# Kernel tuning notes

Measured on AMD Instinct MI355X. Metric: run time of the kernel, lower is better.

The kernel has to match this reference:

```python
import jax, jax.numpy as jnp
import numpy as np

B, S, D, H = 2, 2048, 1024, 16
HD = D // H  # head_dim = 64


def setup_inputs() -> dict:
    key = jax.random.key(0)
    ks = jax.random.split(key, 6)
    scale = D ** -0.5
    x = jax.random.normal(ks[0], (B, S, D), dtype=jnp.float32)
    wq = jax.random.normal(ks[1], (D, D), dtype=jnp.float32) * scale
    wk = jax.random.normal(ks[2], (D, D), dtype=jnp.float32) * scale
    wv = jax.random.normal(ks[3], (D, D), dtype=jnp.float32) * scale
    wo = jax.random.normal(ks[4], (D, D), dtype=jnp.float32) * scale
    # RoPE frequencies: theta_i = 10000^(-2i/HD), angles[t, i] = t * theta_i
    inv_freq = 1.0 / (10000.0 ** (np.arange(0, HD, 2, dtype=np.float32) / HD))
    t = np.arange(S, dtype=np.float32)
    angles = np.outer(t, inv_freq)  # [S, HD//2]
    freqs_cos = jnp.asarray(np.cos(angles), dtype=jnp.float32)
    freqs_sin = jnp.asarray(np.sin(angles), dtype=jnp.float32)
    # additive causal mask [1,1,S,S]
    neg = jnp.float32(-1e9)
    mask = jnp.triu(jnp.full((S, S), neg, dtype=jnp.float32), k=1)[None, None]
    return {"x": x, "wq": wq, "wk": wk, "wv": wv, "wo": wo,
            "freqs_cos": freqs_cos, "freqs_sin": freqs_sin,
            "mask": mask, "start_pos": 0}


def _apply_rope(q, freqs_cos, freqs_sin):
    # q: [B, S, H, HD] -> pairs (even, odd) rotated by angle per position
    b, s, h, hd = q.shape
    q2 = q.reshape(b, s, h, hd // 2, 2)
    qr, qi = q2[..., 0], q2[..., 1]
    c = freqs_cos[None, :, None, :]  # [1, S, 1, HD//2]
    sn = freqs_sin[None, :, None, :]
    out_r = qr * c - qi * sn
    out_i = qr * sn + qi * c
    return jnp.stack([out_r, out_i], axis=-1).reshape(b, s, h, hd)


def reference(x, wq, wk, wv, wo, freqs_cos, freqs_sin, mask, start_pos):
    b, s, _ = x.shape
    xq = (x @ wq).reshape(b, s, H, HD)
    xk = (x @ wk).reshape(b, s, H, HD)
    xv = (x @ wv).reshape(b, s, H, HD)
    xq = _apply_rope(xq, freqs_cos, freqs_sin)
    xk = _apply_rope(xk, freqs_cos, freqs_sin)
    # [B, H, S, HD]
    q = xq.transpose(0, 2, 1, 3)
    k = xk.transpose(0, 2, 1, 3)
    v = xv.transpose(0, 2, 1, 3)
    scores = jnp.einsum('bhqd,bhkd->bhqk', q, k) / jnp.sqrt(jnp.float32(HD))
    scores = scores + mask
    probs = jax.nn.softmax(scores.astype(jnp.float32), axis=-1).astype(q.dtype)
    out = jnp.einsum('bhqk,bhkd->bhqd', probs, v)
    out = out.transpose(0, 2, 1, 3).reshape(b, s, H * HD)
    return out @ wo
```

## Files before the change

kernel.cpp:

```cpp
#include <hip/hip_runtime.h>

typedef unsigned short u16;
typedef __bf16 bf16x8 __attribute__((ext_vector_type(8)));
typedef float f32x4 __attribute__((ext_vector_type(4)));

#define DD 1024
#define SS 2048
#define HH 16
#define HDIM 64

#define VMCNT(N) asm volatile("s_waitcnt vmcnt(" #N ")" ::: "memory")
#define LGKMCNT0 asm volatile("s_waitcnt lgkmcnt(0)" ::: "memory")
#define MEMFENCE asm volatile("" ::: "memory")
#define SBAR __builtin_amdgcn_s_barrier()

__device__ __forceinline__ u16 f2bf(float f) {
  union { float f; unsigned u; } x; x.f = f;
  unsigned r = x.u + 0x7FFFu + ((x.u >> 16) & 1u);
  return (u16)(r >> 16);
}

__device__ __forceinline__ u16 f2bf_s(float f) {
  unsigned r;
  asm("v_cvt_pk_bf16_f32 %0, %1, %2" : "=v"(r) : "v"(f), "v"(0.f));
  return (u16)r;
}

__device__ __forceinline__ void gload_lds16(const u16* g, u16* l) {
  __builtin_amdgcn_global_load_lds((const __attribute__((address_space(1))) void*)g,
                                   (__attribute__((address_space(3))) void*)l, 16, 0, 0);
}

__global__ __launch_bounds__(256) void prep(const float* __restrict__ x,
                                            const float* __restrict__ w0, const float* __restrict__ w1,
                                            const float* __restrict__ w2, const float* __restrict__ w3,
                                            u16* __restrict__ xb, u16* __restrict__ wT) {
  __shared__ float t[32][33];
  const int id = blockIdx.x;
  const int tid = threadIdx.x;
  if (id < 4096) {
    int i = (id * 256 + tid) * 4;
    float4 v = *(const float4*)(x + i);
    xb[i + 0] = f2bf(v.x);
    xb[i + 1] = f2bf(v.y);
    xb[i + 2] = f2bf(v.z);
    xb[i + 3] = f2bf(v.w);
    return;
  }
  const int tt = id - 4096;
  const int z = tt >> 10;
  const int xy = tt & 1023;
  const int j0 = (xy & 31) * 32;
  const int i0 = (xy >> 5) * 32;
  const float* w = (z == 0) ? w0 : (z == 1) ? w1 : (z == 2) ? w2 : w3;
  u16* o = wT + (size_t)z * DD * DD;
  const int tx = tid & 31, ty = tid >> 5;
#pragma unroll
  for (int r = ty; r < 32; r += 8)
    t[r][tx] = w[(size_t)(i0 + r) * DD + j0 + tx];
  __syncthreads();
#pragma unroll
  for (int r = ty; r < 32; r += 8)
    o[(size_t)(j0 + r) * DD + i0 + tx] = f2bf(t[tx][r]);
}

__global__ __launch_bounds__(512, 4) void gemm_qkv(const u16* __restrict__ xb, const u16* __restrict__ wT,
                                                   const float* __restrict__ fc, const float* __restrict__ fs,
                                                   u16* __restrict__ Qr, u16* __restrict__ Kr, u16* __restrict__ Vt) {
  __shared__ u16 As[2][128 * 64];
  __shared__ u16 Bs[2][192 * 64];
  const int tid = threadIdx.x;
  const int lane = tid & 63, wid = tid >> 6;
  const int wm = wid >> 2, wn = wid & 3;
  const int lr = lane & 15, lg = lane >> 4;
  const int m0 = blockIdx.x * 128, n0 = blockIdx.y * 192;

  f32x4 acc[4][3];
#pragma unroll
  for (int i = 0; i < 4; ++i)
#pragma unroll
    for (int j = 0; j < 3; ++j) acc[i][j] = (f32x4){0.f, 0.f, 0.f, 0.f};

  auto stage = [&](int buf, int k0) {
#pragma unroll
    for (int i = 0; i < 2; ++i) {
      int c = tid + i * 512;
      int row = c >> 3, j = (c & 7) ^ (row & 7);
      gload_lds16(xb + (size_t)(m0 + row) * DD + k0 + j * 8, &As[buf][c * 8]);
    }
#pragma unroll
    for (int i = 0; i < 3; ++i) {
      int c = tid + i * 512;
      int row = c >> 3, j = (c & 7) ^ (row & 7);
      gload_lds16(wT + (size_t)(n0 + row) * DD + k0 + j * 8, &Bs[buf][c * 8]);
    }
  };

  stage(0, 0);
  for (int kt = 0; kt < 16; ++kt) {
    const int cur = kt & 1;
    LGKMCNT0; SBAR;
    if (kt < 15) {
      stage(cur ^ 1, (kt + 1) * 64);
      VMCNT(5);
    } else {
      VMCNT(0);
    }
    SBAR; MEMFENCE;
#pragma unroll
    for (int ks = 0; ks < 2; ++ks) {
      bf16x8 af[4], bfr[3];
#pragma unroll
      for (int mi = 0; mi < 4; ++mi) {
        int row = wm * 64 + mi * 16 + lr;
        int ch = (ks * 4 + lg) ^ (row & 7);
        af[mi] = *(const bf16x8*)(&As[cur][row * 64 + ch * 8]);
      }
#pragma unroll
      for (int ni = 0; ni < 3; ++ni) {
        int row = wn * 48 + ni * 16 + lr;
        int ch = (ks * 4 + lg) ^ (row & 7);
        bfr[ni] = *(const bf16x8*)(&Bs[cur][row * 64 + ch * 8]);
      }
      __builtin_amdgcn_s_setprio(1);
#pragma unroll
      for (int mi = 0; mi < 4; ++mi)
#pragma unroll
        for (int ni = 0; ni < 3; ++ni)
          acc[mi][ni] = __builtin_amdgcn_mfma_f32_16x16x32_bf16(af[mi], bfr[ni], acc[mi][ni], 0, 0, 0);
      __builtin_amdgcn_s_setprio(0);
    }
  }

#pragma unroll
  for (int mi = 0; mi < 4; ++mi)
#pragma unroll
    for (int ni = 0; ni < 3; ++ni) {
      const int nb = n0 + wn * 48 + ni * 16;
      const int z = nb >> 10;
      const int nn = (nb & 1023) + lr;
      const int h = nn >> 6, hd = nn & 63;
#pragma unroll
      for (int j = 0; j < 4; ++j) {
        int m = m0 + wm * 64 + mi * 16 + lg * 4 + j;
        float v = acc[mi][ni][j];
        int b = m >> 11, s = m & 2047;
        if (z == 2) {
          Vt[((size_t)(b * HH + h) * HDIM + hd) * SS + s] = f2bf(v);
        } else {
          float pv = __shfl_xor(v, 1);
          int fi = s * 32 + (hd >> 1);
          float c = fc[fi], sn = fs[fi];
          float o = ((hd & 1) == 0) ? (v * c - pv * sn) : (pv * sn + v * c);
          u16* dst = (z == 0) ? Qr : Kr;
          dst[((size_t)(b * HH + h) * SS + s) * HDIM + hd] = f2bf(o);
        }
      }
    }
}

__device__ __forceinline__ void stage_tile(const u16* __restrict__ Kh, const u16* __restrict__ Vh,
                                           int i2, u16* Kbuf, u16* Vbuf, int tid) {
#pragma unroll
  for (int k = 0; k < 2; ++k) {
    const int c = tid + k * 512;
    const int tt = c >> 9, cl = c & 511;
    const int row = cl >> 3, j = (cl & 7) ^ (row & 7);
    gload_lds16(Kh + (size_t)(i2 * 128 + tt * 64 + row) * HDIM + j * 8, Kbuf + c * 8);
    gload_lds16(Vh + (size_t)row * SS + i2 * 128 + tt * 64 + j * 8, Vbuf + c * 8);
  }
}

__device__ __forceinline__ void attn_pass(int qt, int bh, const u16* __restrict__ Qh,
                                          const u16* __restrict__ Kh, const u16* __restrict__ Vh,
                                          u16* __restrict__ Ob, u16* KbR, u16* VbR, u16* Pw,
                                          int gid, int wq) {
  const int tid = threadIdx.x;
  const int lane = tid & 63;
  const int lr = lane & 15, lg = lane >> 4;
  const int q0 = qt * 64 + wq * 16;

  bf16x8 aq[2];
#pragma unroll
  for (int ks = 0; ks < 2; ++ks)
    aq[ks] = *(const bf16x8*)(Qh + (q0 + lr) * HDIM + ks * 32 + lg * 8);

  bf16x8 ones;
  {
    union { u16 u[8]; bf16x8 v; } ou;
#pragma unroll
    for (int i = 0; i < 8; ++i) ou.u[i] = 0x3F80;
    ones = ou.v;
  }

  f32x4 o[4];
#pragma unroll
  for (int d = 0; d < 4; ++d) o[d] = (f32x4){0.f, 0.f, 0.f, 0.f};
  f32x4 ls = (f32x4){0.f, 0.f, 0.f, 0.f};

  const int n2 = (qt + 2) >> 1;

  __syncthreads();
  stage_tile(Kh, Vh, 0, KbR, VbR, tid);

  for (int i = 0; i < n2; ++i) {
    const int cur = i & 1;
    LGKMCNT0; SBAR;
    if (i + 1 < n2) {
      stage_tile(Kh, Vh, i + 1, KbR + (cur ^ 1) * 8192, VbR + (cur ^ 1) * 8192, tid);
      VMCNT(4);
    } else {
      VMCNT(0);
    }
    SBAR; MEMFENCE;

    const int t = 2 * i + gid;
    const u16* Kt = KbR + cur * 8192 + gid * 4096;
    const u16* Vtl = VbR + cur * 8192 + gid * 4096;

    f32x4 sc[4];
#pragma unroll
    for (int kb = 0; kb < 4; ++kb) sc[kb] = (f32x4){0.f, 0.f, 0.f, 0.f};
    __builtin_amdgcn_s_setprio(1);
#pragma unroll
    for (int ks = 0; ks < 2; ++ks)
#pragma unroll
      for (int kb = 0; kb < 4; ++kb) {
        int row = kb * 16 + lr;
        int ch = (ks * 4 + lg) ^ (row & 7);
        bf16x8 bk = *(const bf16x8*)(Kt + row * 64 + ch * 8);
        sc[kb] = __builtin_amdgcn_mfma_f32_16x16x32_bf16(aq[ks], bk, sc[kb], 0, 0, 0);
      }
    __builtin_amdgcn_s_setprio(0);

    if (t >= qt) {
#pragma unroll
      for (int kb = 0; kb < 4; ++kb)
#pragma unroll
        for (int j = 0; j < 4; ++j) {
          int q = q0 + lg * 4 + j;
          int kk = t * 64 + kb * 16 + lr;
          float e = __expf(sc[kb][j] * 0.125f);
          sc[kb][j] = (kk > q) ? 0.f : e;
        }
    } else {
#pragma unroll
      for (int kb = 0; kb < 4; ++kb)
#pragma unroll
        for (int j = 0; j < 4; ++j)
          sc[kb][j] = __expf(sc[kb][j] * 0.125f);
    }

#pragma unroll
    for (int kb = 0; kb < 4; ++kb)
#pragma unroll
      for (int j = 0; j < 4; ++j) {
        int rr = lg * 4 + j;
        int ccol = kb * 16 + lr;
        int ch = (ccol >> 3) ^ (rr & 7);
        Pw[rr * 64 + ch * 8 + (ccol & 7)] = f2bf_s(sc[kb][j]);
      }
#pragma unroll
    for (int ks = 0; ks < 2; ++ks) {
      int chp = (ks * 4 + lg) ^ (lr & 7);
      bf16x8 ap = *(const bf16x8*)(Pw + lr * 64 + chp * 8);
      __builtin_amdgcn_s_setprio(1);
      ls = __builtin_amdgcn_mfma_f32_16x16x32_bf16(ap, ones, ls, 0, 0, 0);
#pragma unroll
      for (int d = 0; d < 4; ++d) {
        int row = d * 16 + lr;
        int ch = (ks * 4 + lg) ^ (row & 7);
        bf16x8 bv = *(const bf16x8*)(Vtl + row * 64 + ch * 8);
        o[d] = __builtin_amdgcn_mfma_f32_16x16x32_bf16(ap, bv, o[d], 0, 0, 0);
      }
      __builtin_amdgcn_s_setprio(0);
    }
  }

  __syncthreads();
  float* mo = (float*)KbR;
  float* ml = (float*)VbR;
  if (gid == 1) {
#pragma unroll
    for (int d = 0; d < 4; ++d)
#pragma unroll
      for (int j = 0; j < 4; ++j)
        mo[(wq * 16 + lg * 4 + j) * 64 + d * 16 + lr] = o[d][j];
    if (lr == 0) {
#pragma unroll
      for (int j = 0; j < 4; ++j) ml[wq * 16 + lg * 4 + j] = ls[j];
    }
  }
  __syncthreads();
  if (gid == 0) {
    const int b = bh >> 4, h = bh & 15;
#pragma unroll
    for (int j = 0; j < 4; ++j) ls[j] += ml[wq * 16 + lg * 4 + j];
#pragma unroll
    for (int d = 0; d < 4; ++d)
#pragma unroll
      for (int j = 0; j < 4; ++j) {
        float val = o[d][j] + mo[(wq * 16 + lg * 4 + j) * 64 + d * 16 + lr];
        int s = q0 + lg * 4 + j;
        int col = h * HDIM + d * 16 + lr;
        Ob[((size_t)b * SS + s) * DD + col] = f2bf(val / ls[j]);
      }
  }
}

__global__ __launch_bounds__(512, 4) void attn(const u16* __restrict__ Qr, const u16* __restrict__ Kr,
                                               const u16* __restrict__ Vt, u16* __restrict__ Ob) {
  __shared__ u16 Kb[2][2][64 * 64];
  __shared__ u16 Vb[2][2][64 * 64];
  __shared__ u16 Ps[8][16 * 64];
  const int id = blockIdx.x;
  const int xcd = id & 7;
  const int r = id >> 3;
  const int pair = r & 15;
  const int bh = xcd * 4 + (r >> 4);
  const u16* Qh = Qr + (size_t)bh * SS * HDIM;
  const u16* Kh = Kr + (size_t)bh * SS * HDIM;
  const u16* Vh = Vt + (size_t)bh * HDIM * SS;
  const int wid = threadIdx.x >> 6;
  const int gid = wid >> 2, wq = wid & 3;
  u16* Pw = &Ps[wid][0];
  attn_pass(pair, bh, Qh, Kh, Vh, Ob, &Kb[0][0][0], &Vb[0][0][0], Pw, gid, wq);
  attn_pass(31 - pair, bh, Qh, Kh, Vh, Ob, &Kb[0][0][0], &Vb[0][0][0], Pw, gid, wq);
}

__global__ __launch_bounds__(512, 4) void gemm_wo(const u16* __restrict__ Ab, const u16* __restrict__ woT,
                                                  float* __restrict__ out) {
  __shared__ u16 As[2][128 * 64];
  __shared__ u16 Bs[2][128 * 64];
  const int tid = threadIdx.x;
  const int lane = tid & 63, wid = tid >> 6;
  const int wm = wid >> 1, wn = wid & 1;
  const int lr = lane & 15, lg = lane >> 4;
  const int m0 = blockIdx.x * 128, n0 = blockIdx.y * 128;

  f32x4 acc[2][4];
#pragma unroll
  for (int i = 0; i < 2; ++i)
#pragma unroll
    for (int j = 0; j < 4; ++j) acc[i][j] = (f32x4){0.f, 0.f, 0.f, 0.f};

  auto stage = [&](int buf, int k0) {
#pragma unroll
    for (int i = 0; i < 2; ++i) {
      int c = tid + i * 512;
      int row = c >> 3, j = (c & 7) ^ (row & 7);
      gload_lds16(Ab + (size_t)(m0 + row) * DD + k0 + j * 8, &As[buf][c * 8]);
      gload_lds16(woT + (size_t)(n0 + row) * DD + k0 + j * 8, &Bs[buf][c * 8]);
    }
  };

  stage(0, 0);
  for (int kt = 0; kt < 16; ++kt) {
    const int cur = kt & 1;
    LGKMCNT0; SBAR;
    if (kt < 15) {
      stage(cur ^ 1, (kt + 1) * 64);
      VMCNT(4);
    } else {
      VMCNT(0);
    }
    SBAR; MEMFENCE;
#pragma unroll
    for (int ks = 0; ks < 2; ++ks) {
      bf16x8 af[2], bfr[4];
#pragma unroll
      for (int mi = 0; mi < 2; ++mi) {
        int row = wm * 32 + mi * 16 + lr;
        int ch = (ks * 4 + lg) ^ (row & 7);
        af[mi] = *(const bf16x8*)(&As[cur][row * 64 + ch * 8]);
      }
#pragma unroll
      for (int ni = 0; ni < 4; ++ni) {
        int row = wn * 64 + ni * 16 + lr;
        int ch = (ks * 4 + lg) ^ (row & 7);
        bfr[ni] = *(const bf16x8*)(&Bs[cur][row * 64 + ch * 8]);
      }
      __builtin_amdgcn_s_setprio(1);
#pragma unroll
      for (int mi = 0; mi < 2; ++mi)
#pragma unroll
        for (int ni = 0; ni < 4; ++ni)
          acc[mi][ni] = __builtin_amdgcn_mfma_f32_16x16x32_bf16(af[mi], bfr[ni], acc[mi][ni], 0, 0, 0);
      __builtin_amdgcn_s_setprio(0);
    }
  }

#pragma unroll
  for (int mi = 0; mi < 2; ++mi)
#pragma unroll
    for (int ni = 0; ni < 4; ++ni)
#pragma unroll
      for (int j = 0; j < 4; ++j) {
        int m = m0 + wm * 32 + mi * 16 + lg * 4 + j;
        int n = n0 + wn * 64 + ni * 16 + lr;
        out[(size_t)m * DD + n] = acc[mi][ni][j];
      }
}

extern "C" void kernel_launch(void* const* d_in, const int* in_sizes, int n_in,
                              void* d_out, int out_size, void* d_ws, size_t ws_size,
                              hipStream_t stream) {
  const float* x  = (const float*)d_in[0];
  const float* wq = (const float*)d_in[1];
  const float* wk = (const float*)d_in[2];
  const float* wv = (const float*)d_in[3];
  const float* wo = (const float*)d_in[4];
  const float* fc = (const float*)d_in[5];
  const float* fs = (const float*)d_in[6];
  float* out = (float*)d_out;

  char* ws = (char*)d_ws;
  u16* xb = (u16*)(ws);
  u16* wT = (u16*)(ws + (8ull << 20));
  u16* Qr = (u16*)(ws + (16ull << 20));
  u16* Kr = (u16*)(ws + (24ull << 20));
  u16* Vt = (u16*)(ws + (32ull << 20));
  u16* Ob = (u16*)(ws + (40ull << 20));

  prep<<<8192, 256, 0, stream>>>(x, wq, wk, wv, wo, xb, wT);
  gemm_qkv<<<dim3(32, 16), 512, 0, stream>>>(xb, wT, fc, fs, Qr, Kr, Vt);
  attn<<<512, 512, 0, stream>>>(Qr, Kr, Vt, Ob);
  gemm_wo<<<dim3(32, 8), 512, 0, stream>>>(Ob, wT + 3ull * DD * DD, out);
}
```

Measured before the change: 113.4 us.

## Use 256x256 QKV GEMM tiles with quadrant-interleaved LDS reads and MFMA

The QKV projection GEMM moves from 128x192 tiles on a 32x16 grid to 256x256 tiles on a 1-D grid of 192 blocks. Block ids are remapped so neighbouring blocks share tiles in cache. Each wave computes a 128x64 output region in four quadrants, alternating LDS fragment reads with MFMA groups separated by barriers. The next k-tile's loads overlap the whole iteration. This raises arithmetic intensity per staged byte and reduces total global traffic, at the cost of more registers and LDS (occupancy bound drops to 2) and only 192 blocks, which may underfill the 256 CUs.

Result: slower. 131.3 us (+15.8%).

```diff
diff --git a/kernel.cpp b/kernel.cpp
--- a/kernel.cpp
+++ b/kernel.cpp
@@ -64,32 +64,61 @@
     o[(size_t)(j0 + r) * DD + i0 + tx] = f2bf(t[tx][r]);
 }
 
-__global__ __launch_bounds__(512, 4) void gemm_qkv(const u16* __restrict__ xb, const u16* __restrict__ wT,
+#define QKV_READ_A(qm)                                                     \
+  _Pragma("unroll") for (int mi = 0; mi < 4; ++mi) {                       \
+    _Pragma("unroll") for (int ks = 0; ks < 2; ++ks) {                     \
+      int ar = wm * 128 + (qm) * 64 + mi * 16 + lr;                        \
+      int ch = (ks * 4 + lg) ^ (ar & 7);                                   \
+      af[mi][ks] = *(const bf16x8*)(A + ar * 64 + ch * 8);                 \
+    }                                                                      \
+  }
+#define QKV_READ_B(qn)                                                     \
+  _Pragma("unroll") for (int ni = 0; ni < 2; ++ni) {                       \
+    _Pragma("unroll") for (int ks = 0; ks < 2; ++ks) {                     \
+      int br = wn * 64 + (qn) * 32 + ni * 16 + lr;                         \
+      int ch = (ks * 4 + lg) ^ (br & 7);                                   \
+      bfv[ni][ks] = *(const bf16x8*)(B + br * 64 + ch * 8);                \
+    }                                                                      \
+  }
+#define QKV_MFMA(qm, qn)                                                   \
+  __builtin_amdgcn_s_setprio(1);                                           \
+  _Pragma("unroll") for (int mi = 0; mi < 4; ++mi)                         \
+    _Pragma("unroll") for (int ni = 0; ni < 2; ++ni)                       \
+      _Pragma("unroll") for (int ks = 0; ks < 2; ++ks)                     \
+        acc[(qm) * 4 + mi][(qn) * 2 + ni] = __builtin_amdgcn_mfma_f32_16x16x32_bf16( \
+            af[mi][ks], bfv[ni][ks], acc[(qm) * 4 + mi][(qn) * 2 + ni], 0, 0, 0);    \
+  __builtin_amdgcn_s_setprio(0);
+
+__global__ __launch_bounds__(512, 2) void gemm_qkv(const u16* __restrict__ xb, const u16* __restrict__ wT,
                                                    const float* __restrict__ fc, const float* __restrict__ fs,
                                                    u16* __restrict__ Qr, u16* __restrict__ Kr, u16* __restrict__ Vt) {
-  __shared__ u16 As[2][128 * 64];
-  __shared__ u16 Bs[2][192 * 64];
+  __shared__ u16 As[2][256 * 64];
+  __shared__ u16 Bs[2][256 * 64];
   const int tid = threadIdx.x;
   const int lane = tid & 63, wid = tid >> 6;
   const int wm = wid >> 2, wn = wid & 3;
   const int lr = lane & 15, lg = lane >> 4;
-  const int m0 = blockIdx.x * 128, n0 = blockIdx.y * 192;
-
-  f32x4 acc[4][3];
-#pragma unroll
-  for (int i = 0; i < 4; ++i)
-#pragma unroll
-    for (int j = 0; j < 3; ++j) acc[i][j] = (f32x4){0.f, 0.f, 0.f, 0.f};
-
-  auto stage = [&](int buf, int k0) {
-#pragma unroll
-    for (int i = 0; i < 2; ++i) {
+  const int id = blockIdx.x;
+  const int wg = (id & 7) * 24 + (id >> 3);
+  const int bx = wg / 12, by = wg % 12;
+  const int m0 = bx * 256, n0 = by * 256;
+
+  f32x4 acc[8][4];
+#pragma unroll
+  for (int i = 0; i < 8; ++i)
+#pragma unroll
+    for (int j = 0; j < 4; ++j) acc[i][j] = (f32x4){0.f, 0.f, 0.f, 0.f};
+
+  auto stage = [&](int buf, int kt) {
+    const int k0 = kt * 64;
+#pragma unroll
+    for (int i = 0; i < 4; ++i) {
       int c = tid + i * 512;
       int row = c >> 3, j = (c & 7) ^ (row & 7);
       gload_lds16(xb + (size_t)(m0 + row) * DD + k0 + j * 8, &As[buf][c * 8]);
     }
 #pragma unroll
-    for (int i = 0; i < 3; ++i) {
+    for (int i = 0; i < 4; ++i) {
       int c = tid + i * 512;
       int row = c >> 3, j = (c & 7) ^ (row & 7);
       gload_lds16(wT + (size_t)(n0 + row) * DD + k0 + j * 8, &Bs[buf][c * 8]);
@@ -97,53 +126,48 @@
   };
 
   stage(0, 0);
-  for (int kt = 0; kt < 16; ++kt) {
-    const int cur = kt & 1;
-    LGKMCNT0; SBAR;
-    if (kt < 15) {
-      stage(cur ^ 1, (kt + 1) * 64);
-      VMCNT(5);
-    } else {
-      VMCNT(0);
-    }
+  VMCNT(0);
+  SBAR; MEMFENCE;
+
+  for (int t = 0; t < 16; ++t) {
+    const int cur = t & 1;
+    const u16* A = &As[cur][0];
+    const u16* B = &Bs[cur][0];
+    bf16x8 af[4][2], bfv[2][2];
+
+    if (t < 15) stage(cur ^ 1, t + 1);
+    QKV_READ_A(0)
+    QKV_READ_B(0)
+    SBAR;
+    QKV_MFMA(0, 0)
+    SBAR;
+    QKV_READ_B(1)
+    SBAR;
+    QKV_MFMA(0, 1)
+    SBAR;
+    QKV_READ_A(1)
+    SBAR;
+    QKV_MFMA(1, 1)
+    SBAR;
+    QKV_READ_B(0)
+    if (t < 15) { VMCNT(0); }
+    SBAR;
+    QKV_MFMA(1, 0)
     SBAR; MEMFENCE;
-#pragma unroll
-    for (int ks = 0; ks < 2; ++ks) {
-      bf16x8 af[4], bfr[3];
-#pragma unroll
-      for (int mi = 0; mi < 4; ++mi) {
-        int row = wm * 64 + mi * 16 + lr;
-        int ch = (ks * 4 + lg) ^ (row & 7);
-        af[mi] = *(const bf16x8*)(&As[cur][row * 64 + ch * 8]);
-      }
-#pragma unroll
-      for (int ni = 0; ni < 3; ++ni) {
-        int row = wn * 48 + ni * 16 + lr;
-        int ch = (ks * 4 + lg) ^ (row & 7);
-        bfr[ni] = *(const bf16x8*)(&Bs[cur][row * 64 + ch * 8]);
-      }
-      __builtin_amdgcn_s_setprio(1);
-#pragma unroll
-      for (int mi = 0; mi < 4; ++mi)
-#pragma unroll
-        for (int ni = 0; ni < 3; ++ni)
-          acc[mi][ni] = __builtin_amdgcn_mfma_f32_16x16x32_bf16(af[mi], bfr[ni], acc[mi][ni], 0, 0, 0);
-      __builtin_amdgcn_s_setprio(0);
-    }
-  }
-
-#pragma unroll
-  for (int mi = 0; mi < 4; ++mi)
-#pragma unroll
-    for (int ni = 0; ni < 3; ++ni) {
-      const int nb = n0 + wn * 48 + ni * 16;
-      const int z = nb >> 10;
-      const int nn = (nb & 1023) + lr;
+  }
+
+  const int z = n0 >> 10;
+#pragma unroll
+  for (int mi8 = 0; mi8 < 8; ++mi8)
+#pragma unroll
+    for (int nj = 0; nj < 4; ++nj) {
+      const int nb = (n0 & 1023) + wn * 64 + (nj >> 1) * 32 + (nj & 1) * 16;
+      const int nn = nb + lr;
       const int h = nn >> 6, hd = nn & 63;
 #pragma unroll
       for (int j = 0; j < 4; ++j) {
-        int m = m0 + wm * 64 + mi * 16 + lg * 4 + j;
-        float v = acc[mi][ni][j];
+        int m = m0 + wm * 128 + (mi8 >> 2) * 64 + (mi8 & 3) * 16 + lg * 4 + j;
+        float v = acc[mi8][nj][j];
         int b = m >> 11, s = m & 2047;
         if (z == 2) {
           Vt[((size_t)(b * HH + h) * HDIM + hd) * SS + s] = f2bf(v);
@@ -423,7 +447,7 @@
   u16* Ob = (u16*)(ws + (40ull << 20));
 
   prep<<<8192, 256, 0, stream>>>(x, wq, wk, wv, wo, xb, wT);
-  gemm_qkv<<<dim3(32, 16), 512, 0, stream>>>(xb, wT, fc, fs, Qr, Kr, Vt);
+  gemm_qkv<<<192, 512, 0, stream>>>(xb, wT, fc, fs, Qr, Kr, Vt);
   attn<<<512, 512, 0, stream>>>(Qr, Kr, Vt, Ob);
   gemm_wo<<<dim3(32, 8), 512, 0, stream>>>(Ob, wT + 3ull * DD * DD, out);
 }
```
